# Performance work log

Hardware: AMD Instinct MI355X
Metric: run time of the kernel (lower is better)

The kernel has to match this reference:

```python
import jax, jax.numpy as jnp
import numpy as np

B, CV, CP, X, Y, Z = 4, 16, 16, 256, 256, 32
NV, NORIG, NSLOT, D = 100000, 131072, 50, 256
CC = CV + CP  # combined_feature_dim = 32


def _l2norm(x, axis):
    n = jnp.linalg.norm(x, axis=axis, keepdims=True)
    return x / jnp.maximum(n, 1e-12)


def _group_norm(x, gamma, beta, groups=4, eps=1e-5):
    # x: [B, C, L]; normalize over (C//groups, L) per group, like nn.GroupNorm
    b, c, l = x.shape
    xg = x.reshape(b, groups, c // groups, l)
    mu = xg.mean(axis=(2, 3), keepdims=True)
    var = xg.var(axis=(2, 3), keepdims=True)
    xg = (xg - mu) / jnp.sqrt(var + eps)
    return xg.reshape(b, c, l) * gamma[None, :, None] + beta[None, :, None]


def setup_inputs() -> dict:
    key = jax.random.key(0)
    ks = jax.random.split(key, 10)
    voxel_feats_dense = jax.random.normal(ks[0], (B, CV, X, Y, Z), dtype=jnp.float32)
    raw_point_feats = jax.random.normal(ks[1], (B, NV, CP), dtype=jnp.float32)
    slot = jax.random.normal(ks[2], (B, NSLOT, D), dtype=jnp.float32)
    # voxel_coords columns: [:,0] indexes Z, [:,1] indexes Y, [:,2] indexes X
    c0 = jax.random.randint(ks[3], (B, NV), 0, Z)
    c1 = jax.random.randint(ks[4], (B, NV), 0, Y)
    c2 = jax.random.randint(ks[5], (B, NV), 0, X)
    voxel_coords = jnp.stack([c0, c1, c2], axis=-1).astype(jnp.int32)
    # unique scatter targets per batch (voxelizer keeps a subset of raw points)
    point_idxes = jnp.stack([
        jax.random.permutation(jax.random.fold_in(ks[6], i), NORIG)[:NV]
        for i in range(B)
    ]).astype(jnp.int32)
    W1 = jax.random.normal(ks[7], (D, D), dtype=jnp.float32) * 0.05
    b1 = jnp.zeros((D,), jnp.float32)
    gn_gamma = jnp.ones((D,), jnp.float32)
    gn_beta = jnp.zeros((D,), jnp.float32)
    W2 = jax.random.normal(ks[8], (CC, D), dtype=jnp.float32) * 0.05
    b2 = jnp.zeros((CC,), jnp.float32)
    return dict(voxel_feats_dense=voxel_feats_dense, raw_point_feats=raw_point_feats,
                slot=slot, W1=W1, b1=b1, gn_gamma=gn_gamma, gn_beta=gn_beta,
                W2=W2, b2=b2, voxel_coords=voxel_coords, point_idxes=point_idxes,
                n_original=NORIG)


def reference(voxel_feats_dense, raw_point_feats, slot, W1, b1, gn_gamma, gn_beta,
              W2, b2, voxel_coords, point_idxes, n_original):
    b, cv, xd, yd, zd = voxel_feats_dense.shape
    vc = voxel_coords
    # voxel-to-point gather: dense[i, :, vc[:,2], vc[:,1], vc[:,0]].T
    lin = vc[..., 2] * (yd * zd) + vc[..., 1] * zd + vc[..., 0]  # [B, NV]
    flat = voxel_feats_dense.reshape(b, cv, -1)
    interp = jnp.take_along_axis(flat, lin[:, None, :], axis=2)  # [B, CV, NV]
    padded_feats = jnp.concatenate([jnp.transpose(interp, (0, 2, 1)),
                                    raw_point_feats], axis=-1)   # [B, NV, CC]
    # object_mlp on slot.transpose(1,2): conv1d(k=1) -> GroupNorm(4) -> ReLU -> conv1d(k=1)
    st = jnp.transpose(slot, (0, 2, 1))                           # [B, D, NSLOT]
    h = jnp.einsum('oc,bcn->bon', W1, st) + b1[None, :, None]
    h = jax.nn.relu(_group_norm(h, gn_gamma, gn_beta))
    slot_proj = jnp.einsum('oc,bcn->bon', W2, h) + b2[None, :, None]  # [B, CC, NSLOT]
    # cosine similarity mask with temperature 0.05
    mask = jnp.einsum('bnc,bck->bnk', _l2norm(padded_feats, 2),
                      _l2norm(slot_proj, 1)) / 0.05                # [B, NV, NSLOT]
    k = mask.shape[2]
    # scatter back to original point indices (zeros elsewhere)
    scatter = jax.vmap(lambda m, idx: jnp.zeros((n_original, k), m.dtype).at[idx].set(m))(
        mask, point_idxes)                                         # [B, NORIG, NSLOT]
    final = jnp.transpose(scatter.reshape(b * n_original, k), (1, 0))  # [NSLOT, B*NORIG]
    return jax.nn.softmax(final, axis=0)
```

## Files before the change

### kernel.cpp

```cpp
#include <hip/hip_runtime.h>

#define BB     4
#define CVC    16
#define CPC    16
#define CCC    32
#define XD     256
#define YD     256
#define ZD     32
#define NVX    100000
#define NORIG  131072
#define NSLOT  50
#define DD     256
#define XYZ    (XD*YD*ZD)
#define BN     ((size_t)BB*NORIG)

__global__ __launch_bounds__(256) void fill_kernel(int* __restrict__ inv,
                                                   float* __restrict__ stats){
  int i = blockIdx.x*256 + threadIdx.x;
  if (i < (int)BN) inv[i] = -1;
  if (i < 32) stats[i] = 0.f;
}

__global__ __launch_bounds__(256) void scatter_kernel(const int* __restrict__ pidx,
                                                      int* __restrict__ inv){
  int t = blockIdx.x*256 + threadIdx.x;
  if (t < BB*NVX){
    int b = t / NVX;
    int n = t - b*NVX;
    inv[b*NORIG + pidx[t]] = n;
  }
}

__global__ __launch_bounds__(256) void mlp1_kernel(
    const float* __restrict__ slot, const float* __restrict__ W1,
    const float* __restrict__ b1, float* __restrict__ ws_h,
    float* __restrict__ stats){
  int s = blockIdx.x, b = blockIdx.y, d = threadIdx.x;
  __shared__ float sv[DD];
  sv[d] = slot[((size_t)b*NSLOT + s)*DD + d];
  __syncthreads();
  const float4* w1q = (const float4*)(W1 + (size_t)d*DD);
  float acc = b1[d];
  #pragma unroll
  for (int q = 0; q < 64; q++){
    float4 w = w1q[q];
    const float* sp = &sv[q*4];
    acc = fmaf(w.x, sp[0], acc);
    acc = fmaf(w.y, sp[1], acc);
    acc = fmaf(w.z, sp[2], acc);
    acc = fmaf(w.w, sp[3], acc);
  }
  ws_h[((size_t)b*NSLOT + s)*DD + d] = acc;
  float s1 = acc, s2 = acc*acc;
  #pragma unroll
  for (int off = 32; off > 0; off >>= 1){
    s1 += __shfl_down(s1, off, 64);
    s2 += __shfl_down(s2, off, 64);
  }
  if ((d & 63) == 0){
    int g = d >> 6;
    atomicAdd(&stats[(b*4+g)*2+0], s1);
    atomicAdd(&stats[(b*4+g)*2+1], s2);
  }
}

__global__ __launch_bounds__(256) void mlp2_kernel(
    const float* __restrict__ ws_h, const float* __restrict__ stats,
    const float* __restrict__ gamma, const float* __restrict__ beta,
    const float* __restrict__ W2, const float* __restrict__ b2,
    float* __restrict__ slotn){
  int s = blockIdx.x, b = blockIdx.y, d = threadIdx.x;
  float h = ws_h[((size_t)b*NSLOT + s)*DD + d];
  int g = d >> 6;
  float s1 = stats[(b*4+g)*2+0];
  float s2 = stats[(b*4+g)*2+1];
  const float invN = 1.f/3200.f;
  float mean = s1*invN;
  float var  = s2*invN - mean*mean;
  float hn = (h - mean) * rsqrtf(var + 1e-5f) * gamma[d] + beta[d];
  hn = fmaxf(hn, 0.f);
  __shared__ float hsh[DD];
  __shared__ float red[256];
  __shared__ float spo[CCC];
  hsh[d] = hn;
  __syncthreads();
  int o = d & 31, ch = d >> 5;
  const float4* w2q = (const float4*)(W2 + (size_t)o*DD + ch*32);
  float p = 0.f;
  #pragma unroll
  for (int q = 0; q < 8; q++){
    float4 w = w2q[q];
    const float* hp = &hsh[ch*32 + q*4];
    p = fmaf(w.x, hp[0], p);
    p = fmaf(w.y, hp[1], p);
    p = fmaf(w.z, hp[2], p);
    p = fmaf(w.w, hp[3], p);
  }
  red[d] = p;
  __syncthreads();
  if (ch == 0){
    float sp = b2[o];
    #pragma unroll
    for (int c = 0; c < 8; c++) sp += red[c*32 + o];
    spo[o] = sp;
  }
  __syncthreads();
  if (d < CCC){
    float ss = 0.f;
    #pragma unroll
    for (int o2 = 0; o2 < CCC; o2++) ss += spo[o2]*spo[o2];
    float sc = 20.f / fmaxf(sqrtf(ss), 1e-12f);
    slotn[((size_t)b*NSLOT + s)*CCC + d] = spo[d]*sc;
  }
}

__global__ __launch_bounds__(256) void main_kernel(
    const float* __restrict__ vox, const float* __restrict__ raw,
    const int* __restrict__ coords, const int* __restrict__ inv,
    const float* __restrict__ slotn, float* __restrict__ out){
  int b = blockIdx.y;
  int col = blockIdx.x*256 + threadIdx.x;
  int n = inv[b*NORIG + col];
  float r[NSLOT];
  if (n >= 0){
    const int* vc = coords + 3*((size_t)b*NVX + n);
    int c0 = vc[0], c1 = vc[1], c2 = vc[2];
    int lin = c2*(YD*ZD) + c1*ZD + c0;
    const float* vb = vox + (size_t)b*CVC*XYZ + lin;
    float f[CCC];
    #pragma unroll
    for (int c = 0; c < CVC; c++) f[c] = vb[(size_t)c*XYZ];
    const float4* rp = (const float4*)(raw + (size_t)CPC*((size_t)b*NVX + n));
    float4 q0 = rp[0], q1 = rp[1], q2 = rp[2], q3 = rp[3];
    f[16] = q0.x; f[17] = q0.y; f[18] = q0.z; f[19] = q0.w;
    f[20] = q1.x; f[21] = q1.y; f[22] = q1.z; f[23] = q1.w;
    f[24] = q2.x; f[25] = q2.y; f[26] = q2.z; f[27] = q2.w;
    f[28] = q3.x; f[29] = q3.y; f[30] = q3.z; f[31] = q3.w;
    float ss = 0.f;
    #pragma unroll
    for (int i = 0; i < CCC; i++) ss = fmaf(f[i], f[i], ss);
    float invn = 1.f / fmaxf(sqrtf(ss), 1e-12f);
    const float* sb = slotn + (size_t)b*NSLOT*CCC;
    float mx = -1e30f;
    #pragma unroll
    for (int k = 0; k < NSLOT; k++){
      const float4* sp = (const float4*)(sb + k*CCC);
      float acc = 0.f;
      #pragma unroll
      for (int q = 0; q < 8; q++){
        float4 v = sp[q];
        acc = fmaf(f[q*4+0], v.x, acc);
        acc = fmaf(f[q*4+1], v.y, acc);
        acc = fmaf(f[q*4+2], v.z, acc);
        acc = fmaf(f[q*4+3], v.w, acc);
      }
      r[k] = acc * invn;
      mx = fmaxf(mx, r[k]);
    }
    float sum = 0.f;
    #pragma unroll
    for (int k = 0; k < NSLOT; k++){ r[k] = __expf(r[k]-mx); sum += r[k]; }
    float rs = 1.f / sum;
    #pragma unroll
    for (int k = 0; k < NSLOT; k++) r[k] *= rs;
  } else {
    #pragma unroll
    for (int k = 0; k < NSLOT; k++) r[k] = 0.02f;
  }
  float* op = out + (size_t)b*NORIG + col;
  #pragma unroll
  for (int k = 0; k < NSLOT; k++) op[(size_t)k*BN] = r[k];
}

extern "C" void kernel_launch(void* const* d_in, const int* in_sizes, int n_in,
                              void* d_out, int out_size, void* d_ws, size_t ws_size,
                              hipStream_t stream) {
  (void)in_sizes; (void)n_in; (void)out_size; (void)ws_size;
  const float* vox    = (const float*)d_in[0];
  const float* raw    = (const float*)d_in[1];
  const float* slot   = (const float*)d_in[2];
  const float* W1     = (const float*)d_in[3];
  const float* b1     = (const float*)d_in[4];
  const float* gamma  = (const float*)d_in[5];
  const float* beta   = (const float*)d_in[6];
  const float* W2     = (const float*)d_in[7];
  const float* b2     = (const float*)d_in[8];
  const int*   coords = (const int*)d_in[9];
  const int*   pidx   = (const int*)d_in[10];
  float*       out    = (float*)d_out;

  int*   inv   = (int*)d_ws;
  float* stats = (float*)((char*)d_ws + BN*sizeof(int));
  float* slotn = stats + 32;
  float* ws_h  = slotn + (size_t)BB*NSLOT*CCC;

  fill_kernel   <<<dim3((unsigned)((BN + 255)/256)), 256, 0, stream>>>(inv, stats);
  scatter_kernel<<<dim3((BB*NVX + 255)/256),          256, 0, stream>>>(pidx, inv);
  mlp1_kernel   <<<dim3(NSLOT, BB),                   256, 0, stream>>>(slot, W1, b1, ws_h, stats);
  mlp2_kernel   <<<dim3(NSLOT, BB),                   256, 0, stream>>>(ws_h, stats, gamma, beta, W2, b2, slotn);
  main_kernel   <<<dim3(NORIG/256, BB),               256, 0, stream>>>(vox, raw, coords, inv, slotn, out);
}
```

Measured before the change: 787.9 us.

## Stage slot vectors in LDS and recompute logits to cut register pressure

The per-batch normalized slot matrix is copied into shared memory so each dot product reads LDS instead of global memory. The 50-element logit array is gone: a first pass accumulates the softmax denominator without max subtraction, and a second pass recomputes each logit and writes it straight out. Feature vectors are pre-scaled by their inverse norm, loops are only partly unrolled, and launch bounds request 6 blocks per SIMD for higher occupancy. This doubles the dot-product arithmetic and drops the max-subtraction safeguard, which is only safe because the logits are bounded by the temperature of 20.

```diff
diff --git a/kernel.cpp b/kernel.cpp
--- a/kernel.cpp
+++ b/kernel.cpp
@@ -114,24 +114,32 @@
   }
 }
 
-__global__ __launch_bounds__(256) void main_kernel(
+__global__ __launch_bounds__(256, 6) void main_kernel(
     const float* __restrict__ vox, const float* __restrict__ raw,
     const int* __restrict__ coords, const int* __restrict__ inv,
     const float* __restrict__ slotn, float* __restrict__ out){
+  __shared__ float ssl[NSLOT*CCC];
   int b = blockIdx.y;
+  {
+    const float4* src = (const float4*)(slotn + (size_t)b*NSLOT*CCC);
+    float4* dst = (float4*)ssl;
+    #pragma unroll
+    for (int i = threadIdx.x; i < (NSLOT*CCC)/4; i += 256) dst[i] = src[i];
+  }
+  __syncthreads();
   int col = blockIdx.x*256 + threadIdx.x;
   int n = inv[b*NORIG + col];
-  float r[NSLOT];
+  float* op = out + (size_t)b*NORIG + col;
   if (n >= 0){
     const int* vc = coords + 3*((size_t)b*NVX + n);
     int c0 = vc[0], c1 = vc[1], c2 = vc[2];
     int lin = c2*(YD*ZD) + c1*ZD + c0;
     const float* vb = vox + (size_t)b*CVC*XYZ + lin;
     float f[CCC];
-    #pragma unroll
-    for (int c = 0; c < CVC; c++) f[c] = vb[(size_t)c*XYZ];
     const float4* rp = (const float4*)(raw + (size_t)CPC*((size_t)b*NVX + n));
     float4 q0 = rp[0], q1 = rp[1], q2 = rp[2], q3 = rp[3];
+    #pragma unroll
+    for (int c = 0; c < CVC; c++) f[c] = vb[(size_t)c*XYZ];
     f[16] = q0.x; f[17] = q0.y; f[18] = q0.z; f[19] = q0.w;
     f[20] = q1.x; f[21] = q1.y; f[22] = q1.z; f[23] = q1.w;
     f[24] = q2.x; f[25] = q2.y; f[26] = q2.z; f[27] = q2.w;
@@ -140,11 +148,12 @@
     #pragma unroll
     for (int i = 0; i < CCC; i++) ss = fmaf(f[i], f[i], ss);
     float invn = 1.f / fmaxf(sqrtf(ss), 1e-12f);
-    const float* sb = slotn + (size_t)b*NSLOT*CCC;
-    float mx = -1e30f;
-    #pragma unroll
+    #pragma unroll
+    for (int i = 0; i < CCC; i++) f[i] *= invn;
+    float sum = 0.f;
+    #pragma unroll 2
     for (int k = 0; k < NSLOT; k++){
-      const float4* sp = (const float4*)(sb + k*CCC);
+      const float4* sp = (const float4*)(ssl + k*CCC);
       float acc = 0.f;
       #pragma unroll
       for (int q = 0; q < 8; q++){
@@ -154,22 +163,27 @@
         acc = fmaf(f[q*4+2], v.z, acc);
         acc = fmaf(f[q*4+3], v.w, acc);
       }
-      r[k] = acc * invn;
-      mx = fmaxf(mx, r[k]);
+      sum += __expf(acc);
     }
-    float sum = 0.f;
-    #pragma unroll
-    for (int k = 0; k < NSLOT; k++){ r[k] = __expf(r[k]-mx); sum += r[k]; }
     float rs = 1.f / sum;
-    #pragma unroll
-    for (int k = 0; k < NSLOT; k++) r[k] *= rs;
+    #pragma unroll 2
+    for (int k = 0; k < NSLOT; k++){
+      const float4* sp = (const float4*)(ssl + k*CCC);
+      float acc = 0.f;
+      #pragma unroll
+      for (int q = 0; q < 8; q++){
+        float4 v = sp[q];
+        acc = fmaf(f[q*4+0], v.x, acc);
+        acc = fmaf(f[q*4+1], v.y, acc);
+        acc = fmaf(f[q*4+2], v.z, acc);
+        acc = fmaf(f[q*4+3], v.w, acc);
+      }
+      op[(size_t)k*BN] = __expf(acc) * rs;
+    }
   } else {
     #pragma unroll
-    for (int k = 0; k < NSLOT; k++) r[k] = 0.02f;
-  }
-  float* op = out + (size_t)b*NORIG + col;
-  #pragma unroll
-  for (int k = 0; k < NSLOT; k++) op[(size_t)k*BN] = r[k];
+    for (int k = 0; k < NSLOT; k++) op[(size_t)k*BN] = 0.02f;
+  }
 }
 
 extern "C" void kernel_launch(void* const* d_in, const int* in_sizes, int n_in,
```

Measured after the change: 834.3 us. 1.06x slower.

## Transpose voxel grid to channel-last and precompute gather indices in scatter

Applied to the files above, without the earlier changes.

Adds a transpose kernel that rewrites the whole dense voxel grid into channel-last order every call. The main kernel can then read each point's 16 voxel channels as four contiguous float4 loads instead of 16 strided scattered loads. The scatter kernel now stores the linear voxel index next to the point index, so the main kernel no longer reads coords. Softmax drops the max subtraction, since logits are bounded by the temperature-scaled cosine, and writes output directly. The cost is a full read and write of the ~0.5 GB voxel volume, which may outweigh the cheaper gather.

```diff
diff --git a/kernel.cpp b/kernel.cpp
--- a/kernel.cpp
+++ b/kernel.cpp
@@ -13,21 +13,43 @@
 #define DD     256
 #define XYZ    (XD*YD*ZD)
 #define BN     ((size_t)BB*NORIG)
-
-__global__ __launch_bounds__(256) void fill_kernel(int* __restrict__ inv,
+#define F4CHUNKS ((size_t)BB*XYZ*CVC/4)
+
+__global__ __launch_bounds__(256) void fill_kernel(int2* __restrict__ il,
                                                    float* __restrict__ stats){
   int i = blockIdx.x*256 + threadIdx.x;
-  if (i < (int)BN) inv[i] = -1;
+  if (i < (int)BN) il[i] = make_int2(-1, 0);
   if (i < 32) stats[i] = 0.f;
 }
 
 __global__ __launch_bounds__(256) void scatter_kernel(const int* __restrict__ pidx,
-                                                      int* __restrict__ inv){
+                                                      const int* __restrict__ coords,
+                                                      int2* __restrict__ il){
   int t = blockIdx.x*256 + threadIdx.x;
   if (t < BB*NVX){
     int b = t / NVX;
     int n = t - b*NVX;
-    inv[b*NORIG + pidx[t]] = n;
+    const int* vc = coords + 3*(size_t)t;
+    int lin = vc[2]*(YD*ZD) + vc[1]*ZD + vc[0];
+    il[(size_t)b*NORIG + pidx[t]] = make_int2(n, lin);
+  }
+}
+
+__global__ __launch_bounds__(256) void transpose_kernel(
+    const float* __restrict__ vox, float* __restrict__ vtx){
+  size_t stride = (size_t)gridDim.x*256;
+  for (size_t g = (size_t)blockIdx.x*256 + threadIdx.x; g < F4CHUNKS; g += stride){
+    int b  = (int)(g >> 23);
+    int r  = (int)(g & ((1u<<23)-1));
+    int v  = r >> 2;
+    int c0 = (r & 3) << 2;
+    const float* src = vox + ((size_t)b*CVC + c0)*XYZ + v;
+    float4 o;
+    o.x = src[0*(size_t)XYZ];
+    o.y = src[1*(size_t)XYZ];
+    o.z = src[2*(size_t)XYZ];
+    o.w = src[3*(size_t)XYZ];
+    ((float4*)vtx)[g] = o;
   }
 }
 
@@ -115,33 +137,37 @@
 }
 
 __global__ __launch_bounds__(256) void main_kernel(
-    const float* __restrict__ vox, const float* __restrict__ raw,
-    const int* __restrict__ coords, const int* __restrict__ inv,
-    const float* __restrict__ slotn, float* __restrict__ out){
+    const float* __restrict__ vtx, const float* __restrict__ raw,
+    const int2* __restrict__ il, const float* __restrict__ slotn,
+    float* __restrict__ out){
   int b = blockIdx.y;
   int col = blockIdx.x*256 + threadIdx.x;
-  int n = inv[b*NORIG + col];
+  int2 t = il[(size_t)b*NORIG + col];
+  float* op = out + (size_t)b*NORIG + col;
+  int n = t.x;
   float r[NSLOT];
   if (n >= 0){
-    const int* vc = coords + 3*((size_t)b*NVX + n);
-    int c0 = vc[0], c1 = vc[1], c2 = vc[2];
-    int lin = c2*(YD*ZD) + c1*ZD + c0;
-    const float* vb = vox + (size_t)b*CVC*XYZ + lin;
-    float f[CCC];
-    #pragma unroll
-    for (int c = 0; c < CVC; c++) f[c] = vb[(size_t)c*XYZ];
+    const float4* vp = (const float4*)(vtx + ((size_t)b*XYZ + (size_t)t.y)*CVC);
+    float4 v0 = vp[0], v1 = vp[1], v2 = vp[2], v3 = vp[3];
     const float4* rp = (const float4*)(raw + (size_t)CPC*((size_t)b*NVX + n));
     float4 q0 = rp[0], q1 = rp[1], q2 = rp[2], q3 = rp[3];
-    f[16] = q0.x; f[17] = q0.y; f[18] = q0.z; f[19] = q0.w;
-    f[20] = q1.x; f[21] = q1.y; f[22] = q1.z; f[23] = q1.w;
-    f[24] = q2.x; f[25] = q2.y; f[26] = q2.z; f[27] = q2.w;
-    f[28] = q3.x; f[29] = q3.y; f[30] = q3.z; f[31] = q3.w;
+    float f[CCC];
+    f[ 0]=v0.x; f[ 1]=v0.y; f[ 2]=v0.z; f[ 3]=v0.w;
+    f[ 4]=v1.x; f[ 5]=v1.y; f[ 6]=v1.z; f[ 7]=v1.w;
+    f[ 8]=v2.x; f[ 9]=v2.y; f[10]=v2.z; f[11]=v2.w;
+    f[12]=v3.x; f[13]=v3.y; f[14]=v3.z; f[15]=v3.w;
+    f[16]=q0.x; f[17]=q0.y; f[18]=q0.z; f[19]=q0.w;
+    f[20]=q1.x; f[21]=q1.y; f[22]=q1.z; f[23]=q1.w;
+    f[24]=q2.x; f[25]=q2.y; f[26]=q2.z; f[27]=q2.w;
+    f[28]=q3.x; f[29]=q3.y; f[30]=q3.z; f[31]=q3.w;
     float ss = 0.f;
     #pragma unroll
     for (int i = 0; i < CCC; i++) ss = fmaf(f[i], f[i], ss);
     float invn = 1.f / fmaxf(sqrtf(ss), 1e-12f);
+    #pragma unroll
+    for (int i = 0; i < CCC; i++) f[i] *= invn;
     const float* sb = slotn + (size_t)b*NSLOT*CCC;
-    float mx = -1e30f;
+    float sum = 0.f;
     #pragma unroll
     for (int k = 0; k < NSLOT; k++){
       const float4* sp = (const float4*)(sb + k*CCC);
@@ -154,22 +180,16 @@
         acc = fmaf(f[q*4+2], v.z, acc);
         acc = fmaf(f[q*4+3], v.w, acc);
       }
-      r[k] = acc * invn;
-      mx = fmaxf(mx, r[k]);
+      r[k] = __expf(acc);
+      sum += r[k];
     }
-    float sum = 0.f;
-    #pragma unroll
-    for (int k = 0; k < NSLOT; k++){ r[k] = __expf(r[k]-mx); sum += r[k]; }
     float rs = 1.f / sum;
     #pragma unroll
-    for (int k = 0; k < NSLOT; k++) r[k] *= rs;
+    for (int k = 0; k < NSLOT; k++) op[(size_t)k*BN] = r[k]*rs;
   } else {
     #pragma unroll
-    for (int k = 0; k < NSLOT; k++) r[k] = 0.02f;
-  }
-  float* op = out + (size_t)b*NORIG + col;
-  #pragma unroll
-  for (int k = 0; k < NSLOT; k++) op[(size_t)k*BN] = r[k];
+    for (int k = 0; k < NSLOT; k++) op[(size_t)k*BN] = 0.02f;
+  }
 }
 
 extern "C" void kernel_launch(void* const* d_in, const int* in_sizes, int n_in,
@@ -189,14 +209,16 @@
   const int*   pidx   = (const int*)d_in[10];
   float*       out    = (float*)d_out;
 
-  int*   inv   = (int*)d_ws;
-  float* stats = (float*)((char*)d_ws + BN*sizeof(int));
+  int2*  il    = (int2*)d_ws;
+  float* stats = (float*)((char*)d_ws + BN*sizeof(int2));
   float* slotn = stats + 32;
   float* ws_h  = slotn + (size_t)BB*NSLOT*CCC;
-
-  fill_kernel   <<<dim3((unsigned)((BN + 255)/256)), 256, 0, stream>>>(inv, stats);
-  scatter_kernel<<<dim3((BB*NVX + 255)/256),          256, 0, stream>>>(pidx, inv);
-  mlp1_kernel   <<<dim3(NSLOT, BB),                   256, 0, stream>>>(slot, W1, b1, ws_h, stats);
-  mlp2_kernel   <<<dim3(NSLOT, BB),                   256, 0, stream>>>(ws_h, stats, gamma, beta, W2, b2, slotn);
-  main_kernel   <<<dim3(NORIG/256, BB),               256, 0, stream>>>(vox, raw, coords, inv, slotn, out);
-}
+  float* vtx   = ws_h  + (size_t)BB*NSLOT*DD;
+
+  fill_kernel     <<<dim3((unsigned)((BN + 255)/256)), 256, 0, stream>>>(il, stats);
+  scatter_kernel  <<<dim3((BB*NVX + 255)/256),          256, 0, stream>>>(pidx, coords, il);
+  transpose_kernel<<<dim3(8192),                        256, 0, stream>>>(vox, vtx);
+  mlp1_kernel     <<<dim3(NSLOT, BB),                   256, 0, stream>>>(slot, W1, b1, ws_h, stats);
+  mlp2_kernel     <<<dim3(NSLOT, BB),                   256, 0, stream>>>(ws_h, stats, gamma, beta, W2, b2, slotn);
+  main_kernel     <<<dim3(NORIG/256, BB),               256, 0, stream>>>(vtx, raw, il, slotn, out);
+}
```

After: 962.0 us. 1.22x slower.
